# Kernel optimization log

Hardware: AMD Instinct MI355X
Metric: run time of the kernel (lower is better)

## Reference

```python
import jax, jax.numpy as jnp
import numpy as np

NPOINT = 1024
RADIUS = 0.2
NSAMPLE = 32
MLP = (64, 64, 128)
EPS = 1e-5  # torch BatchNorm2d default


def farthest_point_sample(xyz, npoint):
    """xyz: [B,N,3] -> centroid indices [B,npoint] (deterministic start at index 0)."""
    B, N, _ = xyz.shape

    def step(carry, _):
        distance, farthest = carry  # [B,N], [B]
        centroid = jnp.take_along_axis(xyz, farthest[:, None, None], axis=1)  # [B,1,3]
        dist = jnp.sum((xyz - centroid) ** 2, axis=-1)  # [B,N]
        distance = jnp.minimum(distance, dist)
        new_farthest = jnp.argmax(distance, axis=-1)
        return (distance, new_farthest), farthest

    init = (jnp.full((B, N), 1e10, xyz.dtype), jnp.zeros((B,), jnp.int32))
    _, centroids = jax.lax.scan(step, init, None, length=npoint)  # [npoint,B]
    return centroids.T  # [B,npoint]


def ball_query(xyz, new_xyz, radius, nsample):
    """xyz:[B,N,3], new_xyz:[B,M,3] -> group_idx [B,M,nsample]."""
    N = xyz.shape[1]
    # sqrdists[b,m,n] = ||new_xyz[b,m] - xyz[b,n]||^2
    sqrdists = jnp.sum((new_xyz[:, :, None, :] - xyz[:, None, :, :]) ** 2, axis=-1)  # [B,M,N]
    idx = jnp.where(sqrdists > radius * radius, N, jnp.arange(N, dtype=jnp.int32))
    idx = jnp.sort(idx, axis=-1)[:, :, :nsample]
    return jnp.where(idx == N, 0, idx)  # out-of-ball slots fall back to point 0 (as in source)


def index_points(points, idx):
    """points:[B,N,C], idx:[B,M,K] -> [B,M,K,C]."""
    B, M, K = idx.shape
    flat = idx.reshape(B, M * K)
    out = jnp.take_along_axis(points, flat[:, :, None], axis=1)
    return out.reshape(B, M, K, points.shape[-1])


def _forward(xyz, points, layers):
    B = xyz.shape[0]
    fps_idx = farthest_point_sample(xyz, NPOINT)
    new_xyz = jnp.take_along_axis(xyz, fps_idx[:, :, None], axis=1)  # [B,M,3]
    group_idx = ball_query(xyz, new_xyz, RADIUS, NSAMPLE)  # [B,M,K]
    grouped_xyz = index_points(xyz, group_idx) - new_xyz[:, :, None, :]  # [B,M,K,3]
    x = jnp.concatenate([grouped_xyz, index_points(points, group_idx)], axis=-1)  # [B,M,K,3+C]
    # shared MLP: 1x1 conv + BatchNorm (training-mode batch stats) + ReLU
    for (w, b, g, be) in layers:
        x = jnp.einsum('bmkc,oc->bmko', x, w) + b
        mean = jnp.mean(x, axis=(0, 1, 2))
        var = jnp.var(x, axis=(0, 1, 2))  # biased, matches torch BN normalization
        x = jax.nn.relu(g * (x - mean) * jax.lax.rsqrt(var + EPS) + be)
    new_points = jnp.max(x, axis=2)  # [B,M,Cout]
    return new_xyz, new_points


def setup_inputs() -> dict:
    key = jax.random.key(0)
    ks = jax.random.split(key, 2 + len(MLP))
    B, N, C = 16, 4096, 64
    inp = {
        'xyz': jax.random.uniform(ks[0], (B, N, 3), jnp.float32),
        'points': jax.random.normal(ks[1], (B, N, C), jnp.float32),
    }
    last = 3 + C
    for i, out_ch in enumerate(MLP):
        inp[f'w{i}'] = jax.random.normal(ks[2 + i], (out_ch, last), jnp.float32) / np.sqrt(last).astype(np.float32)
        inp[f'b{i}'] = jnp.zeros((out_ch,), jnp.float32)
        inp[f'g{i}'] = jnp.ones((out_ch,), jnp.float32)
        inp[f'be{i}'] = jnp.zeros((out_ch,), jnp.float32)
        last = out_ch
    return inp


def reference(xyz, points, w0, b0, g0, be0, w1, b1, g1, be1, w2, b2, g2, be2):
    layers = [(w0, b0, g0, be0), (w1, b1, g1, be1), (w2, b2, g2, be2)]
    return _forward(xyz, points, layers)
```

## Files before the change

### kernel.cpp

```cpp
#include <hip/hip_runtime.h>

typedef unsigned int uint;
typedef unsigned short ushort;
typedef unsigned long long u64;

#define N_PTS 4096
#define B_SZ 16
#define M_PTS 1024
#define K_SMP 32
#define NROWS (B_SZ*M_PTS*K_SMP)
#define INV_CNT (1.0f/524288.0f)

__device__ __forceinline__ float sqdist3(float ax,float ay,float az,float bx,float by,float bz){
  float dx=__fsub_rn(ax,bx), dy=__fsub_rn(ay,by), dz=__fsub_rn(az,bz);
  return __fadd_rn(__fadd_rn(__fmul_rn(dx,dx),__fmul_rn(dy,dy)),__fmul_rn(dz,dz));
}
__device__ __forceinline__ ushort f2bf(float x){
  uint u = __float_as_uint(x);
  u = (u + 0x7fffu + ((u>>16)&1u)) >> 16;
  return (ushort)u;
}
__device__ __forceinline__ float bf2f(uint u){ return __uint_as_float(u<<16); }

template<int CTRL>
__device__ __forceinline__ uint dppu(uint v){
  return (uint)__builtin_amdgcn_update_dpp((int)v, (int)v, CTRL, 0xf, 0xf, false);
}
template<int CTRL>
__device__ __forceinline__ float dppmaxf(float v){
  float o = __uint_as_float(dppu<CTRL>(__float_as_uint(v)));
  return fmaxf(v, o);
}
template<int CTRL>
__device__ __forceinline__ void dppscan(float& v, uint& i){
  float ov = __uint_as_float(dppu<CTRL>(__float_as_uint(v)));
  uint  oi = dppu<CTRL>(i);
  bool tk = (ov >= v);
  v = tk ? ov : v;
  i = tk ? oi : i;
}

__global__ __launch_bounds__(512, 2) void fps_kernel(const float* __restrict__ xyz,
                                                     float* __restrict__ out_newxyz){
  const int b = blockIdx.x;
  const int t = threadIdx.x;
  __shared__ float4 sxyz[N_PTS];
  __shared__ __align__(8) uint2 xch[2][8];
  const float* src = xyz + (size_t)b*N_PTS*3;
  for (int i = t; i < N_PTS; i += 512)
    sxyz[i] = make_float4(src[3*i], src[3*i+1], src[3*i+2], 0.f);
  const int p0 = t*8;
  float px[8], py[8], pz[8], dist[8];
  {
    const float4* s4 = (const float4*)(src + 3*p0);
    float4 v[6];
#pragma unroll
    for (int q=0;q<6;q++) v[q] = s4[q];
    const float* f = (const float*)v;
#pragma unroll
    for (int i=0;i<8;i++){
      px[i]=f[3*i]; py[i]=f[3*i+1]; pz[i]=f[3*i+2];
      dist[i]=1e10f;
    }
  }
  __syncthreads();
  float cx, cy, cz;
  { float4 c0 = sxyz[0]; cx=c0.x; cy=c0.y; cz=c0.z; }
  const int w = t >> 6, lane = t & 63;
  float* outx = out_newxyz + (size_t)b*M_PTS*3;
  for (int s = 0; s < M_PTS; ++s){
    if (t == 0){ outx[s*3+0]=cx; outx[s*3+1]=cy; outx[s*3+2]=cz; }
#pragma unroll
    for (int i=0;i<8;i++){
      float d = sqdist3(px[i],py[i],pz[i],cx,cy,cz);
      dist[i] = fminf(dist[i], d);
    }
    float m8 = fmaxf(fmaxf(fmaxf(dist[0],dist[1]), fmaxf(dist[2],dist[3])),
                     fmaxf(fmaxf(dist[4],dist[5]), fmaxf(dist[6],dist[7])));
    uint li = 7;
    if (dist[6] == m8) li = 6;
    if (dist[5] == m8) li = 5;
    if (dist[4] == m8) li = 4;
    if (dist[3] == m8) li = 3;
    if (dist[2] == m8) li = 2;
    if (dist[1] == m8) li = 1;
    if (dist[0] == m8) li = 0;
    const uint gi = (uint)p0 + li;
    float wm = m8;
    wm = dppmaxf<0x111>(wm);
    wm = dppmaxf<0x112>(wm);
    wm = dppmaxf<0x114>(wm);
    wm = dppmaxf<0x118>(wm);
    wm = dppmaxf<0x142>(wm);
    wm = dppmaxf<0x143>(wm);
    const float M = __uint_as_float((uint)__builtin_amdgcn_readlane((int)__float_as_uint(wm), 63));
    unsigned long long blt = __ballot(m8 == M);
    const int ll = __builtin_ctzll(blt);
    const uint widx = (uint)__builtin_amdgcn_readlane((int)gi, ll);
    const int par = s & 1;
    if (lane == 63) xch[par][w] = make_uint2(__float_as_uint(M), widx);
    __syncthreads();
    uint2 cw = xch[par][lane & 7];
    float cv = __uint_as_float(cw.x); uint ci = cw.y;
    dppscan<0x111>(cv, ci);
    dppscan<0x112>(cv, ci);
    dppscan<0x114>(cv, ci);
    uint fi = (uint)__builtin_amdgcn_readlane((int)ci, 7);
    float4 cc = sxyz[fi];
    cx = cc.x; cy = cc.y; cz = cc.z;
  }
}

__global__ __launch_bounds__(256) void ballq_kernel(const float* __restrict__ xyz,
                                                    const float* __restrict__ newxyz,
                                                    int* __restrict__ gidx){
  const int blk = blockIdx.x;
  const int b = blk >> 6;
  const int mbase = (blk & 63) * 16;
  __shared__ float sx[N_PTS], sy[N_PTS], sz[N_PTS];
  const float* src = xyz + (size_t)b*N_PTS*3;
  for (int i = threadIdx.x; i < N_PTS*3; i += 256){
    float v = src[i]; int p = i/3, j = i%3;
    (j==0?sx:(j==1?sy:sz))[p] = v;
  }
  __syncthreads();
  const int w = threadIdx.x >> 6, lane = threadIdx.x & 63;
  const float R2 = (float)(0.2*0.2);
  for (int mm = w; mm < 16; mm += 4){
    const int m = mbase + mm;
    const float* c = newxyz + ((size_t)b*M_PTS + m)*3;
    float cx = c[0], cy = c[1], cz = c[2];
    int* gout = gidx + ((size_t)b*M_PTS + m)*K_SMP;
    int cnt = 0;
    for (int base = 0; base < N_PTS && cnt < K_SMP; base += 64){
      int p = base + lane;
      float d = sqdist3(sx[p],sy[p],sz[p],cx,cy,cz);
      bool in = (d <= R2);
      unsigned long long mask = __ballot(in);
      int prefix = __popcll(mask & ((1ull << lane) - 1ull));
      int slot = cnt + prefix;
      if (in && slot < K_SMP) gout[slot] = p;
      cnt += __popcll(mask);
    }
    if (cnt < K_SMP){
      int slot = cnt + lane;
      if (slot < K_SMP) gout[slot] = 0;
    }
  }
}

__device__ __forceinline__ void conv_stats64(float s[4], float q[4], float (*sred)[16][8],
                                             int tid, float* S, float* SS){
  const int lane = tid & 63, w = tid >> 6, tc = tid & 15;
#pragma unroll
  for (int j=0;j<4;j++){
    s[j] += __shfl_xor(s[j], 16); s[j] += __shfl_xor(s[j], 32);
    q[j] += __shfl_xor(q[j], 16); q[j] += __shfl_xor(q[j], 32);
  }
  if (lane < 16){
#pragma unroll
    for (int j=0;j<4;j++){ sred[w][tc][j] = s[j]; sred[w][tc][4+j] = q[j]; }
  }
  __syncthreads();
  if (tid < 64){
    const int tcg = tid >> 2, j = tid & 3;
    float a = sred[0][tcg][j]   + sred[1][tcg][j]   + sred[2][tcg][j]   + sred[3][tcg][j];
    float b = sred[0][tcg][4+j] + sred[1][tcg][4+j] + sred[2][tcg][4+j] + sred[3][tcg][4+j];
    atomicAdd(&S[tid], a); atomicAdd(&SS[tid], b);
  }
}

__global__ __launch_bounds__(256, 2) void conv0_kernel(const float* __restrict__ xyz,
                                                       const float* __restrict__ points,
                                                       const float* __restrict__ newxyz,
                                                       const int* __restrict__ gidx,
                                                       const float* __restrict__ W0,
                                                       const float* __restrict__ b0,
                                                       ushort* __restrict__ x1,
                                                       float* __restrict__ S0,
                                                       float* __restrict__ SS0){
  __shared__ float A [67][132];
  __shared__ float Bw[67][68];
  __shared__ float sb[64];
  __shared__ float sred[4][16][8];
  const int tid = threadIdx.x;
  if (tid < 64) sb[tid] = b0[tid];
  for (int idx = tid; idx < 64*67; idx += 256){
    int o = idx / 67, k = idx - o*67;
    Bw[k][o] = W0[idx];
  }
  const size_t rbase = (size_t)blockIdx.x * 128;
  {
    const int r  = tid & 127;
    const int hf = tid >> 7;
    const int R = (int)rbase + r;
    const int b_ = R >> 15, m_ = (R >> 5) & 1023;
    const int g_ = gidx[R];
    const float4* p4 = (const float4*)(points + (((size_t)(b_<<12) + g_) << 6) + hf*32);
#pragma unroll
    for (int j=0;j<8;j++){
      float4 v = p4[j];
      int c = 3 + hf*32 + j*4;
      A[c+0][r]=v.x; A[c+1][r]=v.y; A[c+2][r]=v.z; A[c+3][r]=v.w;
    }
    if (hf == 0){
      const float* pc = newxyz + ((size_t)(b_<<10) + m_)*3;
      const float* pp = xyz    + ((size_t)(b_<<12) + g_)*3;
      A[0][r] = pp[0]-pc[0];
      A[1][r] = pp[1]-pc[1];
      A[2][r] = pp[2]-pc[2];
    }
  }
  __syncthreads();
  const int tr = tid >> 4, tc = tid & 15;
  float acc[8][4];
#pragma unroll
  for (int i=0;i<8;i++)
#pragma unroll
    for (int j=0;j<4;j++) acc[i][j] = sb[tc*4+j];
#pragma unroll 4
  for (int k=0;k<67;k++){
    float4 a0 = *(const float4*)&A [k][tr*8];
    float4 a1 = *(const float4*)&A [k][tr*8+4];
    float4 w  = *(const float4*)&Bw[k][tc*4];
    float av[8] = {a0.x,a0.y,a0.z,a0.w,a1.x,a1.y,a1.z,a1.w};
#pragma unroll
    for (int i=0;i<8;i++){
      acc[i][0]=fmaf(av[i],w.x,acc[i][0]);
      acc[i][1]=fmaf(av[i],w.y,acc[i][1]);
      acc[i][2]=fmaf(av[i],w.z,acc[i][2]);
      acc[i][3]=fmaf(av[i],w.w,acc[i][3]);
    }
  }
  float s[4] = {0.f,0.f,0.f,0.f}, q[4] = {0.f,0.f,0.f,0.f};
#pragma unroll
  for (int i=0;i<8;i++){
    uint2 v;
    v.x = (uint)f2bf(acc[i][0]) | ((uint)f2bf(acc[i][1])<<16);
    v.y = (uint)f2bf(acc[i][2]) | ((uint)f2bf(acc[i][3])<<16);
    *(uint2*)(x1 + ((rbase + tr*8 + i) << 6) + tc*4) = v;
    float v0=bf2f(v.x&0xffffu), v1=bf2f(v.x>>16), v2=bf2f(v.y&0xffffu), v3=bf2f(v.y>>16);
    s[0]+=v0; q[0]=fmaf(v0,v0,q[0]);
    s[1]+=v1; q[1]=fmaf(v1,v1,q[1]);
    s[2]+=v2; q[2]=fmaf(v2,v2,q[2]);
    s[3]+=v3; q[3]=fmaf(v3,v3,q[3]);
  }
  __syncthreads();
  conv_stats64(s, q, sred, tid, S0, SS0);
}

__global__ __launch_bounds__(256, 2) void convg64_kernel(const ushort* __restrict__ xin,
                                                         const float* __restrict__ Sv,
                                                         const float* __restrict__ SSv,
                                                         const float* __restrict__ gg,
                                                         const float* __restrict__ be,
                                                         const float* __restrict__ W,
                                                         const float* __restrict__ bias,
                                                         ushort* __restrict__ xout,
                                                         float* __restrict__ S1,
                                                         float* __restrict__ SS1){
  __shared__ float A [64][132];
  __shared__ float Bw[64][68];
  __shared__ float sc[64], sh[64], sb[64];
  __shared__ float sred[4][16][8];
  const int tid = threadIdx.x;
  if (tid < 64){
    int c = tid;
    float mean = Sv[c]*INV_CNT;
    float var  = fmaf(-mean, mean, SSv[c]*INV_CNT);
    float is   = rsqrtf(var + 1e-5f);
    float scv  = gg[c]*is;
    sc[c] = scv; sh[c] = fmaf(-mean, scv, be[c]);
    sb[c] = bias[c];
  }
  {
    const int o  = tid & 63;
    const int kq = tid >> 6;
    const float* wrow = W + (size_t)o*64 + kq*16;
#pragma unroll
    for (int q=0;q<4;q++){
      float4 wv = *(const float4*)(wrow + q*4);
      int k = kq*16 + q*4;
      Bw[k+0][o]=wv.x; Bw[k+1][o]=wv.y; Bw[k+2][o]=wv.z; Bw[k+3][o]=wv.w;
    }
  }
  __syncthreads();
  const size_t rbase = (size_t)blockIdx.x * 128;
  {
    const int r  = tid & 127;
    const int kh = tid >> 7;
    const uint4* src = (const uint4*)(xin + ((rbase + r) << 6) + kh*32);
#pragma unroll
    for (int g=0; g<4; g++){
      uint4 v = src[g];
      uint d[4] = {v.x,v.y,v.z,v.w};
#pragma unroll
      for (int q=0;q<4;q++){
        int k = kh*32 + g*8 + 2*q;
        float a0 = bf2f(d[q] & 0xffffu), a1 = bf2f(d[q] >> 16);
        A[k+0][r] = fmaxf(fmaf(a0, sc[k+0], sh[k+0]), 0.f);
        A[k+1][r] = fmaxf(fmaf(a1, sc[k+1], sh[k+1]), 0.f);
      }
    }
  }
  __syncthreads();
  const int tr = tid >> 4, tc = tid & 15;
  float acc[8][4];
#pragma unroll
  for (int i=0;i<8;i++)
#pragma unroll
    for (int j=0;j<4;j++) acc[i][j] = sb[tc*4+j];
#pragma unroll 4
  for (int k=0;k<64;k++){
    float4 a0 = *(const float4*)&A [k][tr*8];
    float4 a1 = *(const float4*)&A [k][tr*8+4];
    float4 w  = *(const float4*)&Bw[k][tc*4];
    float av[8] = {a0.x,a0.y,a0.z,a0.w,a1.x,a1.y,a1.z,a1.w};
#pragma unroll
    for (int i=0;i<8;i++){
      acc[i][0]=fmaf(av[i],w.x,acc[i][0]);
      acc[i][1]=fmaf(av[i],w.y,acc[i][1]);
      acc[i][2]=fmaf(av[i],w.z,acc[i][2]);
      acc[i][3]=fmaf(av[i],w.w,acc[i][3]);
    }
  }
  float s[4] = {0.f,0.f,0.f,0.f}, q[4] = {0.f,0.f,0.f,0.f};
#pragma unroll
  for (int i=0;i<8;i++){
    uint2 v;
    v.x = (uint)f2bf(acc[i][0]) | ((uint)f2bf(acc[i][1])<<16);
    v.y = (uint)f2bf(acc[i][2]) | ((uint)f2bf(acc[i][3])<<16);
    *(uint2*)(xout + ((rbase + tr*8 + i) << 6) + tc*4) = v;
    float v0=bf2f(v.x&0xffffu), v1=bf2f(v.x>>16), v2=bf2f(v.y&0xffffu), v3=bf2f(v.y>>16);
    s[0]+=v0; q[0]=fmaf(v0,v0,q[0]);
    s[1]+=v1; q[1]=fmaf(v1,v1,q[1]);
    s[2]+=v2; q[2]=fmaf(v2,v2,q[2]);
    s[3]+=v3; q[3]=fmaf(v3,v3,q[3]);
  }
  __syncthreads();
  conv_stats64(s, q, sred, tid, S1, SS1);
}

__global__ __launch_bounds__(256, 2) void convg128_kernel(const ushort* __restrict__ xin,
                                                          const float* __restrict__ Sv,
                                                          const float* __restrict__ SSv,
                                                          const float* __restrict__ gg,
                                                          const float* __restrict__ be,
                                                          const float* __restrict__ W,
                                                          const float* __restrict__ bias,
                                                          ushort* __restrict__ xout){
  __shared__ float A [64][132];
  __shared__ float Bw[64][132];
  __shared__ float sc[64], sh[64], sb[128];
  const int tid = threadIdx.x;
  if (tid < 64){
    int c = tid;
    float mean = Sv[c]*INV_CNT;
    float var  = fmaf(-mean, mean, SSv[c]*INV_CNT);
    float is   = rsqrtf(var + 1e-5f);
    float scv  = gg[c]*is;
    sc[c] = scv; sh[c] = fmaf(-mean, scv, be[c]);
  }
  if (tid < 128) sb[tid] = bias[tid];
  {
    const int o  = tid & 127;
    const int kh = tid >> 7;
    const float* wrow = W + (size_t)o*64 + kh*32;
#pragma unroll
    for (int q=0;q<8;q++){
      float4 wv = *(const float4*)(wrow + q*4);
      int k = kh*32 + q*4;
      Bw[k+0][o]=wv.x; Bw[k+1][o]=wv.y; Bw[k+2][o]=wv.z; Bw[k+3][o]=wv.w;
    }
  }
  __syncthreads();
  const size_t rbase = (size_t)blockIdx.x * 128;
  {
    const int r  = tid & 127;
    const int kh = tid >> 7;
    const uint4* src = (const uint4*)(xin + ((rbase + r) << 6) + kh*32);
#pragma unroll
    for (int g=0; g<4; g++){
      uint4 v = src[g];
      uint d[4] = {v.x,v.y,v.z,v.w};
#pragma unroll
      for (int q=0;q<4;q++){
        int k = kh*32 + g*8 + 2*q;
        float a0 = bf2f(d[q] & 0xffffu), a1 = bf2f(d[q] >> 16);
        A[k+0][r] = fmaxf(fmaf(a0, sc[k+0], sh[k+0]), 0.f);
        A[k+1][r] = fmaxf(fmaf(a1, sc[k+1], sh[k+1]), 0.f);
      }
    }
  }
  __syncthreads();
  const int tr = tid >> 4, tc = tid & 15;
  float acc[8][8];
#pragma unroll
  for (int i=0;i<8;i++)
#pragma unroll
    for (int j=0;j<8;j++) acc[i][j] = sb[tc*8+j];
#pragma unroll 2
  for (int k=0;k<64;k++){
    float4 a0 = *(const float4*)&A [k][tr*8];
    float4 a1 = *(const float4*)&A [k][tr*8+4];
    float4 w0 = *(const float4*)&Bw[k][tc*8];
    float4 w1 = *(const float4*)&Bw[k][tc*8+4];
    float av[8] = {a0.x,a0.y,a0.z,a0.w,a1.x,a1.y,a1.z,a1.w};
    float wv[8] = {w0.x,w0.y,w0.z,w0.w,w1.x,w1.y,w1.z,w1.w};
#pragma unroll
    for (int i=0;i<8;i++)
#pragma unroll
      for (int j=0;j<8;j++)
        acc[i][j] = fmaf(av[i], wv[j], acc[i][j]);
  }
#pragma unroll
  for (int i=0;i<8;i++){
    uint4 v;
    v.x = (uint)f2bf(acc[i][0]) | ((uint)f2bf(acc[i][1])<<16);
    v.y = (uint)f2bf(acc[i][2]) | ((uint)f2bf(acc[i][3])<<16);
    v.z = (uint)f2bf(acc[i][4]) | ((uint)f2bf(acc[i][5])<<16);
    v.w = (uint)f2bf(acc[i][6]) | ((uint)f2bf(acc[i][7])<<16);
    *(uint4*)(xout + ((rbase + tr*8 + i) << 7) + tc*8) = v;
  }
}

template<int C>
__global__ __launch_bounds__(256) void stats_kernel(const ushort* __restrict__ x,
                                                    float* __restrict__ S,
                                                    float* __restrict__ SS){
  constexpr int GRP = C/8;
  constexpr int RL  = 256/GRP;
  const int cg = threadIdx.x % GRP;
  const int rl = threadIdx.x / GRP;
  const int rows_per_block = NROWS / 1024;
  const int r0 = blockIdx.x * rows_per_block;
  float s[8], ss[8];
#pragma unroll
  for (int j=0;j<8;j++){ s[j]=0.f; ss[j]=0.f; }
  for (int r = r0 + rl; r < r0 + rows_per_block; r += RL){
    uint4 v = *(const uint4*)(x + (size_t)r*C + cg*8);
    uint d[4] = {v.x, v.y, v.z, v.w};
#pragma unroll
    for (int q=0;q<4;q++){
      float a0 = bf2f(d[q] & 0xffffu), a1 = bf2f(d[q] >> 16);
      s[2*q]   += a0; ss[2*q]   = fmaf(a0, a0, ss[2*q]);
      s[2*q+1] += a1; ss[2*q+1] = fmaf(a1, a1, ss[2*q+1]);
    }
  }
  __shared__ float ls[256][8], lss[256][8];
#pragma unroll
  for (int j=0;j<8;j++){ ls[threadIdx.x][j]=s[j]; lss[threadIdx.x][j]=ss[j]; }
  __syncthreads();
  if (threadIdx.x < C){
    const int grp = threadIdx.x >> 3, j = threadIdx.x & 7;
    float a = 0.f, q2 = 0.f;
#pragma unroll
    for (int q = 0; q < RL; q++){ a += ls[q*GRP + grp][j]; q2 += lss[q*GRP + grp][j]; }
    atomicAdd(&S[threadIdx.x], a); atomicAdd(&SS[threadIdx.x], q2);
  }
}

__global__ __launch_bounds__(256) void maxpool_kernel(const ushort* __restrict__ x3,
                                                      const float* __restrict__ S2,
                                                      const float* __restrict__ SS2,
                                                      const float* __restrict__ g2,
                                                      const float* __restrict__ be2,
                                                      float* __restrict__ outp){
  const int lane = threadIdx.x & 63, wv = threadIdx.x >> 6;
  const int bm = blockIdx.x*4 + wv;
  const int c0 = lane*2, c1 = c0+1;
  float mean0 = S2[c0]*INV_CNT;
  float var0  = fmaf(-mean0, mean0, SS2[c0]*INV_CNT);
  float s0 = g2[c0]*rsqrtf(var0+1e-5f);
  float h0 = fmaf(-mean0, s0, be2[c0]);
  float mean1 = S2[c1]*INV_CNT;
  float var1  = fmaf(-mean1, mean1, SS2[c1]*INV_CNT);
  float s1 = g2[c1]*rsqrtf(var1+1e-5f);
  float h1 = fmaf(-mean1, s1, be2[c1]);
  const uint* rb = (const uint*)(x3 + (size_t)bm*K_SMP*128);
  float mx0 = 0.f, mx1 = 0.f;
#pragma unroll
  for (int k=0;k<K_SMP;k++){
    uint v = rb[k*64 + lane];
    float a0 = bf2f(v & 0xffffu), a1 = bf2f(v >> 16);
    mx0 = fmaxf(mx0, fmaxf(fmaf(a0, s0, h0), 0.f));
    mx1 = fmaxf(mx1, fmaxf(fmaf(a1, s1, h1), 0.f));
  }
  float2* o2 = (float2*)(outp + (size_t)bm*128);
  o2[lane] = make_float2(mx0, mx1);
}

extern "C" void kernel_launch(void* const* d_in, const int* in_sizes, int n_in,
                              void* d_out, int out_size, void* d_ws, size_t ws_size,
                              hipStream_t stream){
  const float* xyz    = (const float*)d_in[0];
  const float* points = (const float*)d_in[1];
  const float* w0  = (const float*)d_in[2];
  const float* b0  = (const float*)d_in[3];
  const float* g0  = (const float*)d_in[4];
  const float* be0 = (const float*)d_in[5];
  const float* w1  = (const float*)d_in[6];
  const float* b1  = (const float*)d_in[7];
  const float* g1  = (const float*)d_in[8];
  const float* be1 = (const float*)d_in[9];
  const float* w2  = (const float*)d_in[10];
  const float* b2  = (const float*)d_in[11];
  const float* g2  = (const float*)d_in[12];
  const float* be2 = (const float*)d_in[13];

  float* out      = (float*)d_out;
  float* newxyz   = out;
  float* outp     = out + (size_t)B_SZ*M_PTS*3;

  char* ws = (char*)d_ws;
  int*   gidx  = (int*)ws;
  float* stats = (float*)(ws + (2u<<20));
  float* S0 = stats,      *SS0 = stats+64;
  float* S1 = stats+128,  *SS1 = stats+192;
  float* S2 = stats+256,  *SS2 = stats+384;
  ushort* x1 = (ushort*)(ws + (4u<<20));
  ushort* x3 = (ushort*)(ws + (4u<<20));
  ushort* x2 = (ushort*)(ws + (4u<<20) + 134217728u);

  hipMemsetAsync(stats, 0, 512*sizeof(float), stream);
  fps_kernel  <<<B_SZ, 512, 0, stream>>>(xyz, newxyz);
  ballq_kernel<<<1024, 256, 0, stream>>>(xyz, newxyz, gidx);
  conv0_kernel<<<NROWS/128, 256, 0, stream>>>(xyz, points, newxyz, gidx, w0, b0, x1, S0, SS0);
  convg64_kernel<<<NROWS/128, 256, 0, stream>>>(x1, S0, SS0, g0, be0, w1, b1, x2, S1, SS1);
  convg128_kernel<<<NROWS/128, 256, 0, stream>>>(x2, S1, SS1, g1, be1, w2, b2, x3);
  stats_kernel<128><<<1024, 256, 0, stream>>>(x3, S2, SS2);
  maxpool_kernel<<<NROWS/128, 256, 0, stream>>>(x3, S2, SS2, g2, be2, outp);
}
```

Before: 1.112 ms.

## Widen FPS to 1024 threads with packed math; move BN stats into separate kernels

The farthest-point-sampling kernel now runs 1024 threads per batch, each owning 4 points instead of 8, and computes distances with packed v_pk_add/v_pk_mul f32 instructions. The cross-wave argmax exchange is widened to 16 waves. Separately, the fused per-channel sum and sum-of-squares accumulation (with atomics) is removed from the conv0 and convg64 epilogues and replaced by standalone stats_kernel passes that reread the bf16 activations. This shortens the serial FPS step chain at the cost of an extra block-wide sync over more waves, and adds two full memory passes over the intermediates.

```diff
diff --git a/kernel.cpp b/kernel.cpp
--- a/kernel.cpp
+++ b/kernel.cpp
@@ -3,6 +3,7 @@
 typedef unsigned int uint;
 typedef unsigned short ushort;
 typedef unsigned long long u64;
+typedef __attribute__((ext_vector_type(2))) float f32x2;
 
 #define N_PTS 4096
 #define B_SZ 16
@@ -21,6 +22,13 @@
   return (ushort)u;
 }
 __device__ __forceinline__ float bf2f(uint u){ return __uint_as_float(u<<16); }
+
+__device__ __forceinline__ f32x2 pk_add(f32x2 a, f32x2 b){
+  f32x2 d; asm("v_pk_add_f32 %0, %1, %2" : "=v"(d) : "v"(a), "v"(b)); return d;
+}
+__device__ __forceinline__ f32x2 pk_mul(f32x2 a, f32x2 b){
+  f32x2 d; asm("v_pk_mul_f32 %0, %1, %2" : "=v"(d) : "v"(a), "v"(b)); return d;
+}
 
 template<int CTRL>
 __device__ __forceinline__ uint dppu(uint v){
@@ -40,28 +48,23 @@
   i = tk ? oi : i;
 }
 
-__global__ __launch_bounds__(512, 2) void fps_kernel(const float* __restrict__ xyz,
-                                                     float* __restrict__ out_newxyz){
+__global__ __launch_bounds__(1024) void fps_kernel(const float* __restrict__ xyz,
+                                                   float* __restrict__ out_newxyz){
   const int b = blockIdx.x;
   const int t = threadIdx.x;
   __shared__ float4 sxyz[N_PTS];
-  __shared__ __align__(8) uint2 xch[2][8];
+  __shared__ __align__(8) uint2 xch[2][16];
   const float* src = xyz + (size_t)b*N_PTS*3;
-  for (int i = t; i < N_PTS; i += 512)
+  for (int i = t; i < N_PTS; i += 1024)
     sxyz[i] = make_float4(src[3*i], src[3*i+1], src[3*i+2], 0.f);
-  const int p0 = t*8;
-  float px[8], py[8], pz[8], dist[8];
+  const int p0 = t*4;
+  f32x2 px01, py01, pz01, px23, py23, pz23, d01, d23;
   {
     const float4* s4 = (const float4*)(src + 3*p0);
-    float4 v[6];
-#pragma unroll
-    for (int q=0;q<6;q++) v[q] = s4[q];
-    const float* f = (const float*)v;
-#pragma unroll
-    for (int i=0;i<8;i++){
-      px[i]=f[3*i]; py[i]=f[3*i+1]; pz[i]=f[3*i+2];
-      dist[i]=1e10f;
-    }
+    float4 v0 = s4[0], v1 = s4[1], v2 = s4[2];
+    px01 = f32x2{v0.x, v0.w}; py01 = f32x2{v0.y, v1.x}; pz01 = f32x2{v0.z, v1.y};
+    px23 = f32x2{v1.z, v2.y}; py23 = f32x2{v1.w, v2.z}; pz23 = f32x2{v2.x, v2.w};
+    d01 = f32x2{1e10f, 1e10f}; d23 = f32x2{1e10f, 1e10f};
   }
   __syncthreads();
   float cx, cy, cz;
@@ -70,23 +73,30 @@
   float* outx = out_newxyz + (size_t)b*M_PTS*3;
   for (int s = 0; s < M_PTS; ++s){
     if (t == 0){ outx[s*3+0]=cx; outx[s*3+1]=cy; outx[s*3+2]=cz; }
-#pragma unroll
-    for (int i=0;i<8;i++){
-      float d = sqdist3(px[i],py[i],pz[i],cx,cy,cz);
-      dist[i] = fminf(dist[i], d);
-    }
-    float m8 = fmaxf(fmaxf(fmaxf(dist[0],dist[1]), fmaxf(dist[2],dist[3])),
-                     fmaxf(fmaxf(dist[4],dist[5]), fmaxf(dist[6],dist[7])));
-    uint li = 7;
-    if (dist[6] == m8) li = 6;
-    if (dist[5] == m8) li = 5;
-    if (dist[4] == m8) li = 4;
-    if (dist[3] == m8) li = 3;
-    if (dist[2] == m8) li = 2;
-    if (dist[1] == m8) li = 1;
-    if (dist[0] == m8) li = 0;
+    const f32x2 ncx = f32x2{-cx,-cx}, ncy = f32x2{-cy,-cy}, ncz = f32x2{-cz,-cz};
+    {
+      f32x2 dx = pk_add(px01, ncx);
+      f32x2 dy = pk_add(py01, ncy);
+      f32x2 dz = pk_add(pz01, ncz);
+      f32x2 d  = pk_add(pk_add(pk_mul(dx,dx), pk_mul(dy,dy)), pk_mul(dz,dz));
+      d01.x = fminf(d01.x, d.x);
+      d01.y = fminf(d01.y, d.y);
+    }
+    {
+      f32x2 dx = pk_add(px23, ncx);
+      f32x2 dy = pk_add(py23, ncy);
+      f32x2 dz = pk_add(pz23, ncz);
+      f32x2 d  = pk_add(pk_add(pk_mul(dx,dx), pk_mul(dy,dy)), pk_mul(dz,dz));
+      d23.x = fminf(d23.x, d.x);
+      d23.y = fminf(d23.y, d.y);
+    }
+    float m4 = fmaxf(fmaxf(d01.x, d01.y), fmaxf(d23.x, d23.y));
+    uint li = 3;
+    if (d23.x == m4) li = 2;
+    if (d01.y == m4) li = 1;
+    if (d01.x == m4) li = 0;
     const uint gi = (uint)p0 + li;
-    float wm = m8;
+    float wm = m4;
     wm = dppmaxf<0x111>(wm);
     wm = dppmaxf<0x112>(wm);
     wm = dppmaxf<0x114>(wm);
@@ -94,18 +104,19 @@
     wm = dppmaxf<0x142>(wm);
     wm = dppmaxf<0x143>(wm);
     const float M = __uint_as_float((uint)__builtin_amdgcn_readlane((int)__float_as_uint(wm), 63));
-    unsigned long long blt = __ballot(m8 == M);
+    unsigned long long blt = __ballot(m4 == M);
     const int ll = __builtin_ctzll(blt);
     const uint widx = (uint)__builtin_amdgcn_readlane((int)gi, ll);
     const int par = s & 1;
     if (lane == 63) xch[par][w] = make_uint2(__float_as_uint(M), widx);
     __syncthreads();
-    uint2 cw = xch[par][lane & 7];
+    uint2 cw = xch[par][lane & 15];
     float cv = __uint_as_float(cw.x); uint ci = cw.y;
     dppscan<0x111>(cv, ci);
     dppscan<0x112>(cv, ci);
     dppscan<0x114>(cv, ci);
-    uint fi = (uint)__builtin_amdgcn_readlane((int)ci, 7);
+    dppscan<0x118>(cv, ci);
+    uint fi = (uint)__builtin_amdgcn_readlane((int)ci, 15);
     float4 cc = sxyz[fi];
     cx = cc.x; cy = cc.y; cz = cc.z;
   }
@@ -149,40 +160,16 @@
   }
 }
 
-__device__ __forceinline__ void conv_stats64(float s[4], float q[4], float (*sred)[16][8],
-                                             int tid, float* S, float* SS){
-  const int lane = tid & 63, w = tid >> 6, tc = tid & 15;
-#pragma unroll
-  for (int j=0;j<4;j++){
-    s[j] += __shfl_xor(s[j], 16); s[j] += __shfl_xor(s[j], 32);
-    q[j] += __shfl_xor(q[j], 16); q[j] += __shfl_xor(q[j], 32);
-  }
-  if (lane < 16){
-#pragma unroll
-    for (int j=0;j<4;j++){ sred[w][tc][j] = s[j]; sred[w][tc][4+j] = q[j]; }
-  }
-  __syncthreads();
-  if (tid < 64){
-    const int tcg = tid >> 2, j = tid & 3;
-    float a = sred[0][tcg][j]   + sred[1][tcg][j]   + sred[2][tcg][j]   + sred[3][tcg][j];
-    float b = sred[0][tcg][4+j] + sred[1][tcg][4+j] + sred[2][tcg][4+j] + sred[3][tcg][4+j];
-    atomicAdd(&S[tid], a); atomicAdd(&SS[tid], b);
-  }
-}
-
 __global__ __launch_bounds__(256, 2) void conv0_kernel(const float* __restrict__ xyz,
                                                        const float* __restrict__ points,
                                                        const float* __restrict__ newxyz,
                                                        const int* __restrict__ gidx,
                                                        const float* __restrict__ W0,
                                                        const float* __restrict__ b0,
-                                                       ushort* __restrict__ x1,
-                                                       float* __restrict__ S0,
-                                                       float* __restrict__ SS0){
+                                                       ushort* __restrict__ x1){
   __shared__ float A [67][132];
   __shared__ float Bw[67][68];
   __shared__ float sb[64];
-  __shared__ float sred[4][16][8];
   const int tid = threadIdx.x;
   if (tid < 64) sb[tid] = b0[tid];
   for (int idx = tid; idx < 64*67; idx += 256){
@@ -232,21 +219,13 @@
       acc[i][3]=fmaf(av[i],w.w,acc[i][3]);
     }
   }
-  float s[4] = {0.f,0.f,0.f,0.f}, q[4] = {0.f,0.f,0.f,0.f};
 #pragma unroll
   for (int i=0;i<8;i++){
     uint2 v;
     v.x = (uint)f2bf(acc[i][0]) | ((uint)f2bf(acc[i][1])<<16);
     v.y = (uint)f2bf(acc[i][2]) | ((uint)f2bf(acc[i][3])<<16);
     *(uint2*)(x1 + ((rbase + tr*8 + i) << 6) + tc*4) = v;
-    float v0=bf2f(v.x&0xffffu), v1=bf2f(v.x>>16), v2=bf2f(v.y&0xffffu), v3=bf2f(v.y>>16);
-    s[0]+=v0; q[0]=fmaf(v0,v0,q[0]);
-    s[1]+=v1; q[1]=fmaf(v1,v1,q[1]);
-    s[2]+=v2; q[2]=fmaf(v2,v2,q[2]);
-    s[3]+=v3; q[3]=fmaf(v3,v3,q[3]);
-  }
-  __syncthreads();
-  conv_stats64(s, q, sred, tid, S0, SS0);
+  }
 }
 
 __global__ __launch_bounds__(256, 2) void convg64_kernel(const ushort* __restrict__ xin,
@@ -256,13 +235,10 @@
                                                          const float* __restrict__ be,
                                                          const float* __restrict__ W,
                                                          const float* __restrict__ bias,
-                                                         ushort* __restrict__ xout,
-                                                         float* __restrict__ S1,
-                                                         float* __restrict__ SS1){
+                                                         ushort* __restrict__ xout){
   __shared__ float A [64][132];
   __shared__ float Bw[64][68];
   __shared__ float sc[64], sh[64], sb[64];
-  __shared__ float sred[4][16][8];
   const int tid = threadIdx.x;
   if (tid < 64){
     int c = tid;
@@ -324,21 +300,13 @@
       acc[i][3]=fmaf(av[i],w.w,acc[i][3]);
     }
   }
-  float s[4] = {0.f,0.f,0.f,0.f}, q[4] = {0.f,0.f,0.f,0.f};
 #pragma unroll
   for (int i=0;i<8;i++){
     uint2 v;
     v.x = (uint)f2bf(acc[i][0]) | ((uint)f2bf(acc[i][1])<<16);
     v.y = (uint)f2bf(acc[i][2]) | ((uint)f2bf(acc[i][3])<<16);
     *(uint2*)(xout + ((rbase + tr*8 + i) << 6) + tc*4) = v;
-    float v0=bf2f(v.x&0xffffu), v1=bf2f(v.x>>16), v2=bf2f(v.y&0xffffu), v3=bf2f(v.y>>16);
-    s[0]+=v0; q[0]=fmaf(v0,v0,q[0]);
-    s[1]+=v1; q[1]=fmaf(v1,v1,q[1]);
-    s[2]+=v2; q[2]=fmaf(v2,v2,q[2]);
-    s[3]+=v3; q[3]=fmaf(v3,v3,q[3]);
-  }
-  __syncthreads();
-  conv_stats64(s, q, sred, tid, S1, SS1);
+  }
 }
 
 __global__ __launch_bounds__(256, 2) void convg128_kernel(const ushort* __restrict__ xin,
@@ -523,10 +491,12 @@
   ushort* x2 = (ushort*)(ws + (4u<<20) + 134217728u);
 
   hipMemsetAsync(stats, 0, 512*sizeof(float), stream);
-  fps_kernel  <<<B_SZ, 512, 0, stream>>>(xyz, newxyz);
+  fps_kernel  <<<B_SZ, 1024, 0, stream>>>(xyz, newxyz);
   ballq_kernel<<<1024, 256, 0, stream>>>(xyz, newxyz, gidx);
-  conv0_kernel<<<NROWS/128, 256, 0, stream>>>(xyz, points, newxyz, gidx, w0, b0, x1, S0, SS0);
-  convg64_kernel<<<NROWS/128, 256, 0, stream>>>(x1, S0, SS0, g0, be0, w1, b1, x2, S1, SS1);
+  conv0_kernel<<<NROWS/128, 256, 0, stream>>>(xyz, points, newxyz, gidx, w0, b0, x1);
+  stats_kernel<64><<<1024, 256, 0, stream>>>(x1, S0, SS0);
+  convg64_kernel<<<NROWS/128, 256, 0, stream>>>(x1, S0, SS0, g0, be0, w1, b1, x2);
+  stats_kernel<64><<<1024, 256, 0, stream>>>(x2, S1, SS1);
   convg128_kernel<<<NROWS/128, 256, 0, stream>>>(x2, S1, SS1, g1, be1, w2, b2, x3);
   stats_kernel<128><<<1024, 256, 0, stream>>>(x3, S2, SS2);
   maxpool_kernel<<<NROWS/128, 256, 0, stream>>>(x3, S2, SS2, g2, be2, outp);
```

Measured after the change: 1.274 ms. 1.15x slower.
